# Performance work log

Hardware: AMD Instinct MI355X
Metric: run time of the kernel (lower is better)

The kernel has to match this reference:

```python
import jax, jax.numpy as jnp
import numpy as np

MARGIN = 0.3
N_GALLERY = 32768
N_BATCH = 1024
D_EMB = 512
N_CLASSES = 1000


def setup_inputs() -> dict:
    key = jax.random.key(0)
    k1, k2, k3, k4 = jax.random.split(key, 4)
    inputs = jax.random.normal(k1, (N_BATCH, D_EMB), dtype=jnp.float32)
    features = jax.random.normal(k2, (N_GALLERY, D_EMB), dtype=jnp.float32)
    feat_labels = jax.random.randint(k3, (N_GALLERY,), 0, N_CLASSES, dtype=jnp.int64 if jax.config.read('jax_enable_x64') else jnp.int32)
    idx = jax.random.randint(k4, (N_BATCH,), 0, N_GALLERY, dtype=feat_labels.dtype)
    # invariant from the original code: idx[i] is in the positive set for targets[i]
    targets = feat_labels[idx]
    return {"inputs": inputs, "features": features, "targets": targets,
            "idx": idx, "feat_labels": feat_labels}


def reference(inputs, features, targets, idx, feat_labels):
    # sim_mat: [n, N] similarity against the gallery bank
    sim = jnp.einsum('nd,Nd->nN', inputs, features)
    n = targets.shape[0]
    # positives: same label in gallery, excluding the sample's own gallery slot
    pos_mask = targets[:, None] == feat_labels[None, :]          # [n, N]
    pos_mask = pos_mask.at[jnp.arange(n), idx].set(False)
    # negatives: every gallery entry with a different label
    neg_mask = targets[:, None] != feat_labels[None, :]          # [n, N]
    pos = jnp.min(jnp.where(pos_mask, sim, jnp.inf), axis=1)     # hardest positive (lowest sim)
    neg = jnp.max(jnp.where(neg_mask, sim, -jnp.inf), axis=1)    # hardest negative (highest sim)
    loss = jnp.maximum(neg - pos + MARGIN, 0.0)
    return jnp.mean(loss)
```

## Files before the change

kernel.cpp:

```cpp
#include <hip/hip_runtime.h>
#include <stdint.h>

#define MARGIN 0.3f
#define M 1024
#define NG 32768
#define K 512
#define BM 128
#define BN 128
#define BK 64
#define NT (NG / BN)
#define NPART (NT * 2)

typedef __attribute__((ext_vector_type(8))) __bf16 bf16x8;
typedef __attribute__((ext_vector_type(4))) float f32x4;
typedef unsigned short ushort_t;
typedef unsigned int uint_t;

static __device__ __forceinline__ ushort_t f2bf(float f) {
    uint_t u = __float_as_uint(f);
    u += 0x7FFFu + ((u >> 16) & 1u);
    return (ushort_t)(u >> 16);
}

__global__ __launch_bounds__(256) void cvt_kernel(const float* __restrict__ src,
                                                  ushort_t* __restrict__ dst, int n8) {
    int i = blockIdx.x * 256 + threadIdx.x;
    if (i >= n8) return;
    const float4* s4 = (const float4*)src;
    float4 a = s4[2 * i];
    float4 b = s4[2 * i + 1];
    uint4 o;
    o.x = (uint_t)f2bf(a.x) | ((uint_t)f2bf(a.y) << 16);
    o.y = (uint_t)f2bf(a.z) | ((uint_t)f2bf(a.w) << 16);
    o.z = (uint_t)f2bf(b.x) | ((uint_t)f2bf(b.y) << 16);
    o.w = (uint_t)f2bf(b.z) | ((uint_t)f2bf(b.w) << 16);
    ((uint4*)dst)[i] = o;
}

static __device__ __forceinline__ void gload_lds16(const void* gptr, void* lptr) {
    __builtin_amdgcn_global_load_lds(
        (const __attribute__((address_space(1))) uint32_t*)(gptr),
        (__attribute__((address_space(3))) uint32_t*)(uintptr_t)(lptr),
        16, 0, 0);
}

__global__ __launch_bounds__(256) void gemm_kernel(
    const ushort_t* __restrict__ A,
    const ushort_t* __restrict__ B,
    const int* __restrict__ targets,
    const int* __restrict__ idxv,
    const int* __restrict__ labels,
    float* __restrict__ pos_part,
    float* __restrict__ neg_part) {

    __shared__ __align__(16) ushort_t sA[BM * BK];
    __shared__ __align__(16) ushort_t sB[BN * BK];
    __shared__ int t_s[BM];
    __shared__ int i_s[BM];
    __shared__ int l_s[BN];

    const int tid = threadIdx.x;
    const int lane = tid & 63;
    const int w = tid >> 6;
    const int wm = w >> 1;
    const int wn = w & 1;
    const int bid = blockIdx.x;
    const int mtile = bid & 7;
    const int ntile = bid >> 3;

    if (tid < BM) {
        t_s[tid] = targets[mtile * BM + tid];
        i_s[tid] = idxv[mtile * BM + tid];
    } else {
        l_s[tid - BM] = labels[ntile * BN + (tid - BM)];
    }

    f32x4 zero = {0.f, 0.f, 0.f, 0.f};
    f32x4 acc[4][4];
#pragma unroll
    for (int a = 0; a < 4; ++a)
#pragma unroll
        for (int b = 0; b < 4; ++b) acc[a][b] = zero;

    const int lrow8 = lane >> 3;
    const int lcol = (lane & 7) * 8;

#pragma unroll 1
    for (int kt = 0; kt < K / BK; ++kt) {
        const int kk = kt * BK;
#pragma unroll
        for (int i = 0; i < 4; ++i) {
            const int c = i * 4 + w;
            const int row = c * 8 + lrow8;
            gload_lds16(&A[(size_t)(mtile * BM + row) * K + kk + lcol], &sA[c * 512]);
            gload_lds16(&B[(size_t)(ntile * BN + row) * K + kk + lcol], &sB[c * 512]);
        }
        __syncthreads();
#pragma unroll
        for (int k2 = 0; k2 < 2; ++k2) {
            bf16x8 av[4], bv[4];
#pragma unroll
            for (int mf = 0; mf < 4; ++mf)
                av[mf] = *(const bf16x8*)&sA[(wm * 64 + mf * 16 + (lane & 15)) * BK + k2 * 32 + (lane >> 4) * 8];
#pragma unroll
            for (int nf = 0; nf < 4; ++nf)
                bv[nf] = *(const bf16x8*)&sB[(wn * 64 + nf * 16 + (lane & 15)) * BK + k2 * 32 + (lane >> 4) * 8];
#pragma unroll
            for (int mf = 0; mf < 4; ++mf)
#pragma unroll
                for (int nf = 0; nf < 4; ++nf)
                    acc[mf][nf] = __builtin_amdgcn_mfma_f32_16x16x32_bf16(av[mf], bv[nf], acc[mf][nf], 0, 0, 0);
        }
        __syncthreads();
    }

    const int l15 = lane & 15;
    const int lhi = lane >> 4;
    int labv[4], jv[4];
#pragma unroll
    for (int nf = 0; nf < 4; ++nf) {
        const int cl = wn * 64 + nf * 16 + l15;
        labv[nf] = l_s[cl];
        jv[nf] = ntile * BN + cl;
    }
#pragma unroll
    for (int mf = 0; mf < 4; ++mf) {
#pragma unroll
        for (int r = 0; r < 4; ++r) {
            const int row_l = wm * 64 + mf * 16 + lhi * 4 + r;
            const int tgt = t_s[row_l];
            const int exc = i_s[row_l];
            float pmin = INFINITY, nmax = -INFINITY;
#pragma unroll
            for (int nf = 0; nf < 4; ++nf) {
                const float v = acc[mf][nf][r];
                const bool same = (labv[nf] == tgt);
                pmin = fminf(pmin, (same && (jv[nf] != exc)) ? v : INFINITY);
                nmax = fmaxf(nmax, same ? -INFINITY : v);
            }
#pragma unroll
            for (int s = 1; s < 16; s <<= 1) {
                pmin = fminf(pmin, __shfl_xor(pmin, s, 64));
                nmax = fmaxf(nmax, __shfl_xor(nmax, s, 64));
            }
            if (l15 == 0) {
                const int row_g = mtile * BM + row_l;
                pos_part[(size_t)row_g * NPART + ntile * 2 + wn] = pmin;
                neg_part[(size_t)row_g * NPART + ntile * 2 + wn] = nmax;
            }
        }
    }
}

__global__ __launch_bounds__(256) void rowred_kernel(const float* __restrict__ pos_part,
                                                     const float* __restrict__ neg_part,
                                                     float* __restrict__ loss) {
    const int row = blockIdx.x;
    const int t = threadIdx.x;
    const float* pp = pos_part + (size_t)row * NPART;
    const float* nn = neg_part + (size_t)row * NPART;
    float p = fminf(pp[t], pp[t + 256]);
    float nx = fmaxf(nn[t], nn[t + 256]);
#pragma unroll
    for (int s = 1; s < 64; s <<= 1) {
        p = fminf(p, __shfl_xor(p, s, 64));
        nx = fmaxf(nx, __shfl_xor(nx, s, 64));
    }
    __shared__ float sp[4], sn[4];
    if ((t & 63) == 0) { sp[t >> 6] = p; sn[t >> 6] = nx; }
    __syncthreads();
    if (t == 0) {
        p = fminf(fminf(sp[0], sp[1]), fminf(sp[2], sp[3]));
        nx = fmaxf(fmaxf(sn[0], sn[1]), fmaxf(sn[2], sn[3]));
        const float l = nx - p + MARGIN;
        loss[row] = l > 0.f ? l : 0.f;
    }
}

__global__ __launch_bounds__(256) void final_kernel(const float* __restrict__ loss,
                                                    float* __restrict__ out) {
    const int t = threadIdx.x;
    float s = loss[t] + loss[t + 256] + loss[t + 512] + loss[t + 768];
#pragma unroll
    for (int sh = 1; sh < 64; sh <<= 1) s += __shfl_xor(s, sh, 64);
    __shared__ float sb[4];
    if ((t & 63) == 0) sb[t >> 6] = s;
    __syncthreads();
    if (t == 0) out[0] = (sb[0] + sb[1] + sb[2] + sb[3]) * (1.0f / 1024.0f);
}

extern "C" void kernel_launch(void* const* d_in, const int* in_sizes, int n_in,
                              void* d_out, int out_size, void* d_ws, size_t ws_size,
                              hipStream_t stream) {
    const float* inputs = (const float*)d_in[0];
    const float* features = (const float*)d_in[1];
    const int* targets = (const int*)d_in[2];
    const int* idxv = (const int*)d_in[3];
    const int* labels = (const int*)d_in[4];

    char* ws = (char*)d_ws;
    ushort_t* A = (ushort_t*)ws;
    ushort_t* B = (ushort_t*)(ws + (1u << 20));
    float* pos_part = (float*)(ws + (1u << 20) + (32u << 20));
    float* neg_part = pos_part + (size_t)M * NPART;
    float* loss = neg_part + (size_t)M * NPART;

    cvt_kernel<<<(NG * K / 8) / 256, 256, 0, stream>>>(features, B, NG * K / 8);
    cvt_kernel<<<(M * K / 8) / 256, 256, 0, stream>>>(inputs, A, M * K / 8);

    gemm_kernel<<<(M / BM) * (NG / BN), 256, 0, stream>>>(A, B, targets, idxv, labels,
                                                          pos_part, neg_part);

    rowred_kernel<<<M, 256, 0, stream>>>(pos_part, neg_part, loss);
    final_kernel<<<1, 256, 0, stream>>>(loss, (float*)d_out);
}
```

Measured before the change: 185.4 us.

## Double-buffer 256x256 GEMM tiles with swizzled LDS and fuse final reduction

Enlarges the GEMM tile to 256x256 with 512 threads. It double-buffers the LDS stages for A and B, uses an XOR-swizzled LDS layout to cut bank conflicts, and raises wave priority around the MFMA bursts. The final mean kernel is dropped: the row-reduce kernel now atomically adds scaled losses into a zeroed output. The aim is more reuse per tile and overlap of global loads with MFMA, paid for with higher register and LDS pressure and a float atomic whose summation order is nondeterministic.

```diff
diff --git a/kernel.cpp b/kernel.cpp
--- a/kernel.cpp
+++ b/kernel.cpp
@@ -5,16 +5,21 @@
 #define M 1024
 #define NG 32768
 #define K 512
-#define BM 128
-#define BN 128
+#define BM 256
+#define BN 256
 #define BK 64
-#define NT (NG / BN)
-#define NPART (NT * 2)
+#define KT (K / BK)
+#define NTILES (NG / BN)
+#define MTILES (M / BM)
+#define NPART (NTILES * 4)
 
 typedef __attribute__((ext_vector_type(8))) __bf16 bf16x8;
 typedef __attribute__((ext_vector_type(4))) float f32x4;
 typedef unsigned short ushort_t;
 typedef unsigned int uint_t;
+
+#define BAR() __builtin_amdgcn_s_barrier()
+#define LGKM0() asm volatile("s_waitcnt lgkmcnt(0)" ::: "memory")
 
 static __device__ __forceinline__ ushort_t f2bf(float f) {
     uint_t u = __float_as_uint(f);
@@ -44,7 +49,7 @@
         16, 0, 0);
 }
 
-__global__ __launch_bounds__(256) void gemm_kernel(
+__global__ __launch_bounds__(512, 2) void gemm_kernel(
     const ushort_t* __restrict__ A,
     const ushort_t* __restrict__ B,
     const int* __restrict__ targets,
@@ -53,8 +58,8 @@
     float* __restrict__ pos_part,
     float* __restrict__ neg_part) {
 
-    __shared__ __align__(16) ushort_t sA[BM * BK];
-    __shared__ __align__(16) ushort_t sB[BN * BK];
+    __shared__ __align__(16) ushort_t sA[2][BM * BK];
+    __shared__ __align__(16) ushort_t sB[2][BN * BK];
     __shared__ int t_s[BM];
     __shared__ int i_s[BM];
     __shared__ int l_s[BN];
@@ -62,11 +67,13 @@
     const int tid = threadIdx.x;
     const int lane = tid & 63;
     const int w = tid >> 6;
-    const int wm = w >> 1;
-    const int wn = w & 1;
+    const int wm = w >> 2;
+    const int wn = w & 3;
+    const int l15 = lane & 15;
+    const int lhi = lane >> 4;
     const int bid = blockIdx.x;
-    const int mtile = bid & 7;
-    const int ntile = bid >> 3;
+    const int ntile = bid & (NTILES - 1);
+    const int mtile = bid >> 7;
 
     if (tid < BM) {
         t_s[tid] = targets[mtile * BM + tid];
@@ -76,46 +83,110 @@
     }
 
     f32x4 zero = {0.f, 0.f, 0.f, 0.f};
-    f32x4 acc[4][4];
-#pragma unroll
-    for (int a = 0; a < 4; ++a)
+    f32x4 acc[8][4];
+#pragma unroll
+    for (int a = 0; a < 8; ++a)
 #pragma unroll
         for (int b = 0; b < 4; ++b) acc[a][b] = zero;
 
-    const int lrow8 = lane >> 3;
-    const int lcol = (lane & 7) * 8;
+    const int rstage = tid >> 3;
+    const int cstage = (((tid & 7) ^ (rstage & 7)) << 3);
+    const ushort_t* Abase = A + (size_t)mtile * BM * K;
+    const ushort_t* Bbase = B + (size_t)ntile * BN * K;
+
+    auto stage_half = [&](const ushort_t* g, ushort_t* l) {
+        gload_lds16(g + (size_t)rstage * K + cstage, l + w * 512);
+        gload_lds16(g + (size_t)(64 + rstage) * K + cstage, l + 4096 + w * 512);
+    };
+
+    auto readA = [&](int buf, int mf, int kk) -> bf16x8 {
+        const int r = wm * 128 + mf * 16 + l15;
+        const int u = (kk * 4 + lhi) ^ (r & 7);
+        return *(const bf16x8*)&sA[buf][r * 64 + u * 8];
+    };
+    auto readB = [&](int buf, int nf, int kk) -> bf16x8 {
+        const int r = wn * 64 + nf * 16 + l15;
+        const int u = (kk * 4 + lhi) ^ (r & 7);
+        return *(const bf16x8*)&sB[buf][r * 64 + u * 8];
+    };
+
+    stage_half(Abase, &sA[0][0]);
+    stage_half(Abase + (size_t)128 * K, &sA[0][8192]);
+    stage_half(Bbase, &sB[0][0]);
+    stage_half(Bbase + (size_t)128 * K, &sB[0][8192]);
+    stage_half(Bbase + BK, &sB[1][0]);
+    stage_half(Bbase + BK + (size_t)128 * K, &sB[1][8192]);
+    asm volatile("s_waitcnt vmcnt(4)" ::: "memory");
+    BAR();
 
 #pragma unroll 1
-    for (int kt = 0; kt < K / BK; ++kt) {
-        const int kk = kt * BK;
-#pragma unroll
-        for (int i = 0; i < 4; ++i) {
-            const int c = i * 4 + w;
-            const int row = c * 8 + lrow8;
-            gload_lds16(&A[(size_t)(mtile * BM + row) * K + kk + lcol], &sA[c * 512]);
-            gload_lds16(&B[(size_t)(ntile * BN + row) * K + kk + lcol], &sB[c * 512]);
+    for (int kt = 0; kt < KT; ++kt) {
+        const int cur = kt & 1;
+        bf16x8 av[4], bv[4];
+
+#pragma unroll
+        for (int nf = 0; nf < 4; ++nf) bv[nf] = readB(cur, nf, 0);
+#pragma unroll
+        for (int mf = 0; mf < 4; ++mf) av[mf] = readA(cur, mf, 0);
+        if (kt < KT - 1) stage_half(Abase + (size_t)(kt + 1) * BK, &sA[cur ^ 1][0]);
+        BAR(); LGKM0();
+        __builtin_amdgcn_s_setprio(1);
+#pragma unroll
+        for (int mf = 0; mf < 4; ++mf)
+#pragma unroll
+            for (int nf = 0; nf < 4; ++nf)
+                acc[mf][nf] = __builtin_amdgcn_mfma_f32_16x16x32_bf16(av[mf], bv[nf], acc[mf][nf], 0, 0, 0);
+        __builtin_amdgcn_s_setprio(0);
+        BAR();
+
+#pragma unroll
+        for (int mf = 0; mf < 4; ++mf) av[mf] = readA(cur, mf + 4, 0);
+        if (kt < KT - 1)
+            stage_half(Abase + (size_t)(kt + 1) * BK + (size_t)128 * K, &sA[cur ^ 1][8192]);
+        BAR(); LGKM0();
+        __builtin_amdgcn_s_setprio(1);
+#pragma unroll
+        for (int mf = 0; mf < 4; ++mf)
+#pragma unroll
+            for (int nf = 0; nf < 4; ++nf)
+                acc[mf + 4][nf] = __builtin_amdgcn_mfma_f32_16x16x32_bf16(av[mf], bv[nf], acc[mf + 4][nf], 0, 0, 0);
+        __builtin_amdgcn_s_setprio(0);
+        BAR();
+
+#pragma unroll
+        for (int nf = 0; nf < 4; ++nf) bv[nf] = readB(cur, nf, 1);
+#pragma unroll
+        for (int mf = 0; mf < 4; ++mf) av[mf] = readA(cur, mf, 1);
+        BAR(); LGKM0();
+        __builtin_amdgcn_s_setprio(1);
+#pragma unroll
+        for (int mf = 0; mf < 4; ++mf)
+#pragma unroll
+            for (int nf = 0; nf < 4; ++nf)
+                acc[mf][nf] = __builtin_amdgcn_mfma_f32_16x16x32_bf16(av[mf], bv[nf], acc[mf][nf], 0, 0, 0);
+        __builtin_amdgcn_s_setprio(0);
+        BAR();
+
+#pragma unroll
+        for (int mf = 0; mf < 4; ++mf) av[mf] = readA(cur, mf + 4, 1);
+        if (kt < KT - 2) {
+            stage_half(Bbase + (size_t)(kt + 2) * BK, &sB[cur][0]);
+            stage_half(Bbase + (size_t)(kt + 2) * BK + (size_t)128 * K, &sB[cur][8192]);
+            asm volatile("s_waitcnt vmcnt(4)" ::: "memory");
+        } else {
+            asm volatile("s_waitcnt vmcnt(0)" ::: "memory");
         }
-        __syncthreads();
-#pragma unroll
-        for (int k2 = 0; k2 < 2; ++k2) {
-            bf16x8 av[4], bv[4];
-#pragma unroll
-            for (int mf = 0; mf < 4; ++mf)
-                av[mf] = *(const bf16x8*)&sA[(wm * 64 + mf * 16 + (lane & 15)) * BK + k2 * 32 + (lane >> 4) * 8];
-#pragma unroll
-            for (int nf = 0; nf < 4; ++nf)
-                bv[nf] = *(const bf16x8*)&sB[(wn * 64 + nf * 16 + (lane & 15)) * BK + k2 * 32 + (lane >> 4) * 8];
-#pragma unroll
-            for (int mf = 0; mf < 4; ++mf)
-#pragma unroll
-                for (int nf = 0; nf < 4; ++nf)
-                    acc[mf][nf] = __builtin_amdgcn_mfma_f32_16x16x32_bf16(av[mf], bv[nf], acc[mf][nf], 0, 0, 0);
-        }
-        __syncthreads();
-    }
-
-    const int l15 = lane & 15;
-    const int lhi = lane >> 4;
+        BAR(); LGKM0();
+        __builtin_amdgcn_s_setprio(1);
+#pragma unroll
+        for (int mf = 0; mf < 4; ++mf)
+#pragma unroll
+            for (int nf = 0; nf < 4; ++nf)
+                acc[mf + 4][nf] = __builtin_amdgcn_mfma_f32_16x16x32_bf16(av[mf], bv[nf], acc[mf + 4][nf], 0, 0, 0);
+        __builtin_amdgcn_s_setprio(0);
+        BAR();
+    }
+
     int labv[4], jv[4];
 #pragma unroll
     for (int nf = 0; nf < 4; ++nf) {
@@ -124,10 +195,10 @@
         jv[nf] = ntile * BN + cl;
     }
 #pragma unroll
-    for (int mf = 0; mf < 4; ++mf) {
+    for (int mf = 0; mf < 8; ++mf) {
 #pragma unroll
         for (int r = 0; r < 4; ++r) {
-            const int row_l = wm * 64 + mf * 16 + lhi * 4 + r;
+            const int row_l = wm * 128 + mf * 16 + lhi * 4 + r;
             const int tgt = t_s[row_l];
             const int exc = i_s[row_l];
             float pmin = INFINITY, nmax = -INFINITY;
@@ -145,8 +216,8 @@
             }
             if (l15 == 0) {
                 const int row_g = mtile * BM + row_l;
-                pos_part[(size_t)row_g * NPART + ntile * 2 + wn] = pmin;
-                neg_part[(size_t)row_g * NPART + ntile * 2 + wn] = nmax;
+                pos_part[(size_t)row_g * NPART + ntile * 4 + wn] = pmin;
+                neg_part[(size_t)row_g * NPART + ntile * 4 + wn] = nmax;
             }
         }
     }
@@ -154,7 +225,7 @@
 
 __global__ __launch_bounds__(256) void rowred_kernel(const float* __restrict__ pos_part,
                                                      const float* __restrict__ neg_part,
-                                                     float* __restrict__ loss) {
+                                                     float* __restrict__ out) {
     const int row = blockIdx.x;
     const int t = threadIdx.x;
     const float* pp = pos_part + (size_t)row * NPART;
@@ -173,20 +244,8 @@
         p = fminf(fminf(sp[0], sp[1]), fminf(sp[2], sp[3]));
         nx = fmaxf(fmaxf(sn[0], sn[1]), fmaxf(sn[2], sn[3]));
         const float l = nx - p + MARGIN;
-        loss[row] = l > 0.f ? l : 0.f;
-    }
-}
-
-__global__ __launch_bounds__(256) void final_kernel(const float* __restrict__ loss,
-                                                    float* __restrict__ out) {
-    const int t = threadIdx.x;
-    float s = loss[t] + loss[t + 256] + loss[t + 512] + loss[t + 768];
-#pragma unroll
-    for (int sh = 1; sh < 64; sh <<= 1) s += __shfl_xor(s, sh, 64);
-    __shared__ float sb[4];
-    if ((t & 63) == 0) sb[t >> 6] = s;
-    __syncthreads();
-    if (t == 0) out[0] = (sb[0] + sb[1] + sb[2] + sb[3]) * (1.0f / 1024.0f);
+        atomicAdd(out, (l > 0.f ? l : 0.f) * (1.0f / (float)M));
+    }
 }
 
 extern "C" void kernel_launch(void* const* d_in, const int* in_sizes, int n_in,
@@ -203,14 +262,14 @@
     ushort_t* B = (ushort_t*)(ws + (1u << 20));
     float* pos_part = (float*)(ws + (1u << 20) + (32u << 20));
     float* neg_part = pos_part + (size_t)M * NPART;
-    float* loss = neg_part + (size_t)M * NPART;
+
+    hipMemsetAsync(d_out, 0, sizeof(float), stream);
 
     cvt_kernel<<<(NG * K / 8) / 256, 256, 0, stream>>>(features, B, NG * K / 8);
     cvt_kernel<<<(M * K / 8) / 256, 256, 0, stream>>>(inputs, A, M * K / 8);
 
-    gemm_kernel<<<(M / BM) * (NG / BN), 256, 0, stream>>>(A, B, targets, idxv, labels,
-                                                          pos_part, neg_part);
-
-    rowred_kernel<<<M, 256, 0, stream>>>(pos_part, neg_part, loss);
-    final_kernel<<<1, 256, 0, stream>>>(loss, (float*)d_out);
-}
+    gemm_kernel<<<MTILES * NTILES, 512, 0, stream>>>(A, B, targets, idxv, labels,
+                                                     pos_part, neg_part);
+
+    rowred_kernel<<<M, 256, 0, stream>>>(pos_part, neg_part, (float*)d_out);
+}
```

Result: faster. 176.3 us (-4.9%).
